# Kernel optimization log

Measured on AMD Instinct MI355X. Metric: run time of the kernel, lower is better.

## Reference

```python
import jax, jax.numpy as jnp
import numpy as np

BS = 8192
NUM_CLASSES = 400
D = 768


def _bilin_from_14(m14, Y, X, eH, eW):
    # Value of bilinear-resize(m14 -> (eH,eW)) at integer pixel (Y,X), computed on the fly.
    # torch F.interpolate(align_corners=False): src = (dst+0.5)*in/out - 0.5, clamped at 0.
    # m14: (bs,14,14); Y,X: (bs,14) float integer-valued coords; eH,eW: (bs,) float.
    sy = jnp.maximum((Y + 0.5) * 14.0 / eH[:, None] - 0.5, 0.0)
    sx = jnp.maximum((X + 0.5) * 14.0 / eW[:, None] - 0.5, 0.0)
    r0f = jnp.floor(sy); c0f = jnp.floor(sx)
    r0 = r0f.astype(jnp.int32); r1 = jnp.minimum(r0 + 1, 13)
    c0 = c0f.astype(jnp.int32); c1 = jnp.minimum(c0 + 1, 13)
    fy = sy - r0f; fx = sx - c0f
    b = jnp.arange(m14.shape[0])[:, None, None]
    g00 = m14[b, r0[:, :, None], c0[:, None, :]]
    g01 = m14[b, r0[:, :, None], c1[:, None, :]]
    g10 = m14[b, r1[:, :, None], c0[:, None, :]]
    g11 = m14[b, r1[:, :, None], c1[:, None, :]]
    wy = fy[:, :, None]; wx = fx[:, None, :]
    return g00 * (1 - wy) * (1 - wx) + g01 * (1 - wy) * wx + g10 * wy * (1 - wx) + g11 * wy * wx


def _get_mask(attn, o_pos, e_pos):
    # Fused, fully-batched equivalent of the per-sample python loop:
    #   resize 14x14 -> (eH,eW) bilinear; crop (top,left,oH,oW); resize -> 14x14 bilinear.
    # The final resize only reads the intermediate grid at 4 integer points per output
    # pixel, so we evaluate those points lazily via _bilin_from_14 (exact, no Emax grid).
    bs = attn.shape[0]
    m14 = attn.reshape(bs, 14, 14)
    eH = e_pos[:, 2].astype(jnp.float32); eW = e_pos[:, 3].astype(jnp.float32)
    top = (o_pos[:, 0] - e_pos[:, 0]).astype(jnp.float32)
    left = (o_pos[:, 1] - e_pos[:, 1]).astype(jnp.float32)
    oH = o_pos[:, 2].astype(jnp.float32); oW = o_pos[:, 3].astype(jnp.float32)
    i = jnp.arange(14, dtype=jnp.float32)[None, :]
    ty = jnp.maximum((i + 0.5) * oH[:, None] / 14.0 - 0.5, 0.0)  # (bs,14) coords in crop
    tx = jnp.maximum((i + 0.5) * oW[:, None] / 14.0 - 0.5, 0.0)
    y0 = jnp.floor(ty); y1 = jnp.minimum(y0 + 1.0, oH[:, None] - 1.0); wy = ty - y0
    x0 = jnp.floor(tx); x1 = jnp.minimum(x0 + 1.0, oW[:, None] - 1.0); wx = tx - x0
    Y0 = top[:, None] + y0; Y1 = top[:, None] + y1  # absolute rows in (eH,eW) grid
    X0 = left[:, None] + x0; X1 = left[:, None] + x1
    v00 = _bilin_from_14(m14, Y0, X0, eH, eW)
    v01 = _bilin_from_14(m14, Y0, X1, eH, eW)
    v10 = _bilin_from_14(m14, Y1, X0, eH, eW)
    v11 = _bilin_from_14(m14, Y1, X1, eH, eW)
    wyc = wy[:, :, None]; wxc = wx[:, None, :]
    out = v00 * (1 - wyc) * (1 - wxc) + v01 * (1 - wyc) * wxc + v10 * wyc * (1 - wxc) + v11 * wyc * wxc
    return out.reshape(bs, 196)


def _get_att_mask(attention, ratio=0.5):
    bs = attention.shape[0]
    a14 = attention.reshape(bs, 14, 14)
    # bilinear 14->7 with align_corners=False samples at frac 0.5 == 2x2 average pool
    a7 = a14.reshape(bs, 7, 2, 7, 2).mean(axis=(2, 4))
    flat = a7.reshape(bs, 49)
    n_keep = int(49 * ratio) + 1  # argsort desc, take top N+1 = 25
    _, idx = jax.lax.top_k(flat, n_keep)
    masks = jnp.ones((bs, 49), dtype=bool)
    masks = masks.at[jnp.arange(bs)[:, None], idx].set(False)
    m7 = masks.reshape(bs, 7, 7)
    full = jnp.repeat(jnp.repeat(m7, 2, axis=1), 2, axis=2)
    return full.reshape(bs, 196)


def setup_inputs() -> dict:
    key = jax.random.key(0)
    k1, k2, k3 = jax.random.split(key, 3)
    attn = jax.random.uniform(k1, (BS, 196), dtype=jnp.float32)
    rng = np.random.default_rng(0)
    IMG = 224
    eH = rng.integers(112, IMG + 1, BS); eW = rng.integers(112, IMG + 1, BS)
    eT = rng.integers(0, IMG - eH + 1); eL = rng.integers(0, IMG - eW + 1)
    def box():
        h = rng.integers(56, eH + 1); w = rng.integers(56, eW + 1)
        t = eT + rng.integers(0, eH - h + 1); l = eL + rng.integers(0, eW - w + 1)
        return np.stack([t, l, h, w], axis=1)
    e = np.stack([eT, eL, eH, eW], axis=1)
    pos = np.stack([box(), box(), e], axis=1).astype(np.int32)  # (BS,3,4)
    image_embed = jax.random.normal(k2, (2 * BS, D), dtype=jnp.float32)
    W = jax.random.normal(k3, (NUM_CLASSES, D), dtype=jnp.float32) * 0.02
    b = jnp.zeros((NUM_CLASSES,), dtype=jnp.float32)
    return {"attn": attn, "pos": jnp.asarray(pos), "image_embed": image_embed, "W": W, "b": b}


def reference(attn, pos, image_embed, W, b):
    cm1 = _get_mask(attn, pos[:, 0], pos[:, 2])
    mask1 = _get_att_mask(cm1)
    cm2 = _get_mask(attn, pos[:, 1], pos[:, 2])
    mask2 = _get_att_mask(cm2)
    mask = jnp.concatenate([mask1, mask2], axis=0)  # (2*bs,196) bool, fed to masked encoder
    logits = image_embed @ W.T + b
    return logits, mask
```

## Files before the change

### kernel.cpp

```cpp
#include <hip/hip_runtime.h>
#include <hip/hip_bf16.h>
#include <stdint.h>
#include <type_traits>

#define BSAMP 8192
#define NCLS 400
#define DIM 768
#define LOGITS_SIZE (16384LL * 400LL)
#define GEMM_BLOCKS 640
#define MASK_BLOCKS 4096
#define W_ELEMS (NCLS * DIM)

typedef __attribute__((ext_vector_type(8))) short short8;
typedef __attribute__((ext_vector_type(4))) float floatx4;

__device__ inline unsigned int packbf(float a, float b) {
    unsigned int ua = __float_as_uint(a) + 0x8000u;
    unsigned int ub = __float_as_uint(b) + 0x8000u;
    return __builtin_amdgcn_perm(ub, ua, 0x07060302u);
}

__device__ inline short8 cvt8(float4 lo, float4 hi) {
    union { unsigned int u[4]; short8 s; } r;
    r.u[0] = packbf(lo.x, lo.y);
    r.u[1] = packbf(lo.z, lo.w);
    r.u[2] = packbf(hi.x, hi.y);
    r.u[3] = packbf(hi.z, hi.w);
    return r.s;
}

__device__ inline void gload16(const void* g, void* l) {
    __builtin_amdgcn_global_load_lds((const __attribute__((address_space(1))) void*)g,
                                     (__attribute__((address_space(3))) void*)l, 16, 0, 0);
}

__global__ void cvtW_kernel(const float* __restrict__ W, unsigned short* __restrict__ ws) {
    int i = (blockIdx.x * 256 + threadIdx.x) * 4;
    if (i < W_ELEMS) {
        float4 f = *(const float4*)(W + i);
        uint2 r;
        r.x = packbf(f.x, f.y);
        r.y = packbf(f.z, f.w);
        *(uint2*)(ws + i) = r;
    }
}

__device__ inline float bilin14(const float* m14, float Y, float X, float eH, float eW) {
    float sy = fmaxf((Y + 0.5f) * 14.0f / eH - 0.5f, 0.0f);
    float sx = fmaxf((X + 0.5f) * 14.0f / eW - 0.5f, 0.0f);
    float r0f = floorf(sy);
    float c0f = floorf(sx);
    int r0 = (int)r0f;
    int r1 = min(r0 + 1, 13);
    int c0 = (int)c0f;
    int c1 = min(c0 + 1, 13);
    float fy = sy - r0f;
    float fx = sx - c0f;
    float g00 = m14[r0 * 14 + c0];
    float g01 = m14[r0 * 14 + c1];
    float g10 = m14[r1 * 14 + c0];
    float g11 = m14[r1 * 14 + c1];
    return g00 * (1.f - fy) * (1.f - fx) + g01 * (1.f - fy) * fx +
           g10 * fy * (1.f - fx) + g11 * fy * fx;
}

struct MaskSm { float m14[4][208]; float a7[4][56]; float mv[4][56]; };

template <bool USE_WS>
struct GemmSm {
    float A[2][128 * 32];
    typename std::conditional<USE_WS, unsigned short, float>::type B[2][80 * 32];
};

template <bool USE_WS>
__global__ __launch_bounds__(256, 2) void fused_kernel(const float* __restrict__ attn,
                                                       const int* __restrict__ pos,
                                                       const float* __restrict__ E,
                                                       const float* __restrict__ W,
                                                       const float* __restrict__ bias,
                                                       const unsigned short* __restrict__ wsW,
                                                       float* __restrict__ out) {
    __shared__ __align__(16) union SmU {
        GemmSm<USE_WS> g;
        MaskSm m;
    } sm;

    const int bx = blockIdx.x;
    const int t  = threadIdx.x;
    const int wv = t >> 6, ln = t & 63;

    if (bx < GEMM_BLOCKS) {
        const int xcd = bx & 7, li = bx >> 3;
        const int band = (li / 5) * 8 + xcd;
        const int n0 = (li % 5) * 80;
        const int m0 = band << 7;
        const int quad = ln >> 4, l16 = ln & 15;

        auto stageA = [&](int k0, float* buf) {
#pragma unroll
            for (int j = 0; j < 4; ++j) {
                int r = wv * 32 + j * 8 + (ln >> 3);
                int c = ln & 7;
                const float* src = E + (size_t)(m0 + r) * DIM + k0 + 4 * (c ^ (r & 7));
                gload16(src, buf + (wv * 32 + j * 8) * 32);
            }
        };
        auto stageBw = [&](int k0, unsigned short* buf) {
            for (int j = wv; j < 5; j += 4) {
                int row = j * 16 + (ln >> 2);
                int c = ln & 3;
                const unsigned short* src = wsW + (size_t)(n0 + row) * DIM + k0 + 8 * (c ^ ((row >> 1) & 3));
                gload16(src, buf + (j * 16) * 32);
            }
        };
        auto stageBf = [&](int k0, float* buf) {
            for (int j = wv; j < 10; j += 4) {
                int r = j * 8 + (ln >> 3);
                int c = ln & 7;
                const float* src = W + (size_t)(n0 + r) * DIM + k0 + 4 * (c ^ (r & 7));
                gload16(src, buf + (j * 8) * 32);
            }
        };
        auto stage = [&](int k0, int buf) {
            stageA(k0, sm.g.A[buf]);
            if constexpr (USE_WS) stageBw(k0, sm.g.B[buf]);
            else stageBf(k0, (float*)sm.g.B[buf]);
        };

        floatx4 acc[2][5];
#pragma unroll
        for (int mi = 0; mi < 2; ++mi)
#pragma unroll
            for (int ni = 0; ni < 5; ++ni)
                acc[mi][ni] = (floatx4){0.f, 0.f, 0.f, 0.f};

        stage(0, 0);
        stage(32, 1);
        __syncthreads();

        for (int it = 0; it < 24; ++it) {
            const int cur = it & 1;
            const float* aS = sm.g.A[cur];

            short8 af[2];
#pragma unroll
            for (int mi = 0; mi < 2; ++mi) {
                int r = wv * 32 + mi * 16 + l16;
                int rx = r & 7;
                const float* rp = aS + r * 32;
                float4 lo = *(const float4*)(rp + (((quad << 1) ^ rx) << 2));
                float4 hi = *(const float4*)(rp + ((((quad << 1) | 1) ^ rx) << 2));
                af[mi] = cvt8(lo, hi);
            }
#pragma unroll
            for (int ni = 0; ni < 5; ++ni) {
                int row = ni * 16 + l16;
                short8 bfr;
                if constexpr (USE_WS) {
                    bfr = *(const short8*)(sm.g.B[cur] + row * 32 + 8 * (quad ^ ((row >> 1) & 3)));
                } else {
                    int rx = row & 7;
                    const float* rp = (const float*)sm.g.B[cur] + row * 32;
                    float4 lo = *(const float4*)(rp + (((quad << 1) ^ rx) << 2));
                    float4 hi = *(const float4*)(rp + ((((quad << 1) | 1) ^ rx) << 2));
                    bfr = cvt8(lo, hi);
                }
                acc[0][ni] = __builtin_amdgcn_mfma_f32_16x16x32_bf16(af[0], bfr, acc[0][ni], 0, 0, 0);
                acc[1][ni] = __builtin_amdgcn_mfma_f32_16x16x32_bf16(af[1], bfr, acc[1][ni], 0, 0, 0);
            }

            __syncthreads();
            if (it < 22) stage((it + 2) * 32, cur);
        }

#pragma unroll
        for (int ni = 0; ni < 5; ++ni) {
            int col = n0 + ni * 16 + l16;
            float bv = bias[col];
#pragma unroll
            for (int mi = 0; mi < 2; ++mi) {
                int rowBase = m0 + wv * 32 + mi * 16 + quad * 4;
#pragma unroll
                for (int r = 0; r < 4; ++r) {
                    out[(size_t)(rowBase + r) * NCLS + col] = acc[mi][ni][r] + bv;
                }
            }
        }
    } else {
        const int p = (bx - GEMM_BLOCKS) * 4 + wv;
        const int b = p & (BSAMP - 1);
        const int o = p >> 13;
        float* m14 = sm.m.m14[wv];

        for (int i = ln; i < 196; i += 64) m14[i] = attn[(size_t)b * 196 + i];

        const int* pb = pos + (size_t)b * 12;
        const float topf  = (float)(pb[o * 4 + 0] - pb[8]);
        const float leftf = (float)(pb[o * 4 + 1] - pb[9]);
        const float oH = (float)pb[o * 4 + 2];
        const float oW = (float)pb[o * 4 + 3];
        const float eH = (float)pb[10];
        const float eW = (float)pb[11];
        __syncthreads();

        const int i7 = ln / 7, j7 = ln - i7 * 7;
        if (ln < 49) {
            float s = 0.f;
#pragma unroll
            for (int dy = 0; dy < 2; ++dy) {
                int oy = 2 * i7 + dy;
                float ty = fmaxf((oy + 0.5f) * oH / 14.0f - 0.5f, 0.0f);
                float y0 = floorf(ty);
                float y1 = fminf(y0 + 1.0f, oH - 1.0f);
                float wy = ty - y0;
                float Y0 = topf + y0, Y1 = topf + y1;
#pragma unroll
                for (int dx = 0; dx < 2; ++dx) {
                    int ox = 2 * j7 + dx;
                    float tx = fmaxf((ox + 0.5f) * oW / 14.0f - 0.5f, 0.0f);
                    float x0 = floorf(tx);
                    float x1 = fminf(x0 + 1.0f, oW - 1.0f);
                    float wx = tx - x0;
                    float X0 = leftf + x0, X1 = leftf + x1;
                    float v00 = bilin14(m14, Y0, X0, eH, eW);
                    float v01 = bilin14(m14, Y0, X1, eH, eW);
                    float v10 = bilin14(m14, Y1, X0, eH, eW);
                    float v11 = bilin14(m14, Y1, X1, eH, eW);
                    float cm = v00 * (1.f - wy) * (1.f - wx) + v01 * (1.f - wy) * wx +
                               v10 * wy * (1.f - wx) + v11 * wy * wx;
                    s += cm;
                }
            }
            sm.m.a7[wv][ln] = s * 0.25f;
        }
        __syncthreads();

        if (ln < 49) {
            float mine = sm.m.a7[wv][ln];
            int cnt = 0;
#pragma unroll 7
            for (int s2 = 0; s2 < 49; ++s2) {
                float v = sm.m.a7[wv][s2];
                cnt += (v > mine) || (v == mine && s2 < ln);
            }
            sm.m.mv[wv][ln] = (cnt < 25) ? 0.0f : 1.0f;
        }
        __syncthreads();

        float* ob = out + LOGITS_SIZE + (size_t)p * 196;
        for (int i = ln; i < 196; i += 64) {
            int oy = i / 14, ox = i - oy * 14;
            ob[i] = sm.m.mv[wv][(oy >> 1) * 7 + (ox >> 1)];
        }
    }
}

extern "C" void kernel_launch(void* const* d_in, const int* in_sizes, int n_in,
                              void* d_out, int out_size, void* d_ws, size_t ws_size,
                              hipStream_t stream) {
    const float* attn = (const float*)d_in[0];
    const int*   pos  = (const int*)d_in[1];
    const float* E    = (const float*)d_in[2];
    const float* W    = (const float*)d_in[3];
    const float* bias = (const float*)d_in[4];
    float* out = (float*)d_out;

    if (ws_size >= (size_t)W_ELEMS * 2) {
        unsigned short* ws = (unsigned short*)d_ws;
        cvtW_kernel<<<300, 256, 0, stream>>>(W, ws);
        fused_kernel<true><<<GEMM_BLOCKS + MASK_BLOCKS, 256, 0, stream>>>(
            attn, pos, E, W, bias, ws, out);
    } else {
        fused_kernel<false><<<GEMM_BLOCKS + MASK_BLOCKS, 256, 0, stream>>>(
            attn, pos, E, W, bias, nullptr, out);
    }
}
```

Baseline: 150.7 us.

## Halve GEMM tile rows to 64 for higher occupancy and hoist mask coordinate math

After: 150.0 us. Within noise of the previous version (-0.5%).

```diff
diff --git a/kernel.cpp b/kernel.cpp
--- a/kernel.cpp
+++ b/kernel.cpp
@@ -7,7 +7,7 @@
 #define NCLS 400
 #define DIM 768
 #define LOGITS_SIZE (16384LL * 400LL)
-#define GEMM_BLOCKS 640
+#define GEMM_BLOCKS 1280
 #define MASK_BLOCKS 4096
 #define W_ELEMS (NCLS * DIM)
 
@@ -45,17 +45,9 @@
     }
 }
 
-__device__ inline float bilin14(const float* m14, float Y, float X, float eH, float eW) {
-    float sy = fmaxf((Y + 0.5f) * 14.0f / eH - 0.5f, 0.0f);
-    float sx = fmaxf((X + 0.5f) * 14.0f / eW - 0.5f, 0.0f);
-    float r0f = floorf(sy);
-    float c0f = floorf(sx);
-    int r0 = (int)r0f;
+__device__ inline float tap4(const float* m14, int r0, int c0, float fy, float fx) {
     int r1 = min(r0 + 1, 13);
-    int c0 = (int)c0f;
     int c1 = min(c0 + 1, 13);
-    float fy = sy - r0f;
-    float fx = sx - c0f;
     float g00 = m14[r0 * 14 + c0];
     float g01 = m14[r0 * 14 + c1];
     float g10 = m14[r1 * 14 + c0];
@@ -68,12 +60,12 @@
 
 template <bool USE_WS>
 struct GemmSm {
-    float A[2][128 * 32];
+    float A[2][64 * 32];
     typename std::conditional<USE_WS, unsigned short, float>::type B[2][80 * 32];
 };
 
 template <bool USE_WS>
-__global__ __launch_bounds__(256, 2) void fused_kernel(const float* __restrict__ attn,
+__global__ __launch_bounds__(256, 6) void fused_kernel(const float* __restrict__ attn,
                                                        const int* __restrict__ pos,
                                                        const float* __restrict__ E,
                                                        const float* __restrict__ W,
@@ -90,19 +82,17 @@
     const int wv = t >> 6, ln = t & 63;
 
     if (bx < GEMM_BLOCKS) {
-        const int xcd = bx & 7, li = bx >> 3;
-        const int band = (li / 5) * 8 + xcd;
-        const int n0 = (li % 5) * 80;
-        const int m0 = band << 7;
+        const int n0 = (bx % 5) * 80;
+        const int m0 = (bx / 5) * 64;
         const int quad = ln >> 4, l16 = ln & 15;
 
         auto stageA = [&](int k0, float* buf) {
 #pragma unroll
-            for (int j = 0; j < 4; ++j) {
-                int r = wv * 32 + j * 8 + (ln >> 3);
+            for (int j = 0; j < 2; ++j) {
+                int r = wv * 16 + j * 8 + (ln >> 3);
                 int c = ln & 7;
                 const float* src = E + (size_t)(m0 + r) * DIM + k0 + 4 * (c ^ (r & 7));
-                gload16(src, buf + (wv * 32 + j * 8) * 32);
+                gload16(src, buf + (wv * 16 + j * 8) * 32);
             }
         };
         auto stageBw = [&](int k0, unsigned short* buf) {
@@ -127,12 +117,9 @@
             else stageBf(k0, (float*)sm.g.B[buf]);
         };
 
-        floatx4 acc[2][5];
-#pragma unroll
-        for (int mi = 0; mi < 2; ++mi)
-#pragma unroll
-            for (int ni = 0; ni < 5; ++ni)
-                acc[mi][ni] = (floatx4){0.f, 0.f, 0.f, 0.f};
+        floatx4 acc[5];
+#pragma unroll
+        for (int ni = 0; ni < 5; ++ni) acc[ni] = (floatx4){0.f, 0.f, 0.f, 0.f};
 
         stage(0, 0);
         stage(32, 1);
@@ -140,17 +127,14 @@
 
         for (int it = 0; it < 24; ++it) {
             const int cur = it & 1;
-            const float* aS = sm.g.A[cur];
-
-            short8 af[2];
-#pragma unroll
-            for (int mi = 0; mi < 2; ++mi) {
-                int r = wv * 32 + mi * 16 + l16;
-                int rx = r & 7;
-                const float* rp = aS + r * 32;
+
+            short8 af;
+            {
+                int rx = l16 & 7;
+                const float* rp = sm.g.A[cur] + (wv * 16 + l16) * 32;
                 float4 lo = *(const float4*)(rp + (((quad << 1) ^ rx) << 2));
                 float4 hi = *(const float4*)(rp + ((((quad << 1) | 1) ^ rx) << 2));
-                af[mi] = cvt8(lo, hi);
+                af = cvt8(lo, hi);
             }
 #pragma unroll
             for (int ni = 0; ni < 5; ++ni) {
@@ -165,25 +149,21 @@
                     float4 hi = *(const float4*)(rp + ((((quad << 1) | 1) ^ rx) << 2));
                     bfr = cvt8(lo, hi);
                 }
-                acc[0][ni] = __builtin_amdgcn_mfma_f32_16x16x32_bf16(af[0], bfr, acc[0][ni], 0, 0, 0);
-                acc[1][ni] = __builtin_amdgcn_mfma_f32_16x16x32_bf16(af[1], bfr, acc[1][ni], 0, 0, 0);
+                acc[ni] = __builtin_amdgcn_mfma_f32_16x16x32_bf16(af, bfr, acc[ni], 0, 0, 0);
             }
 
             __syncthreads();
             if (it < 22) stage((it + 2) * 32, cur);
         }
 
+        const int rowBase = m0 + wv * 16 + quad * 4;
 #pragma unroll
         for (int ni = 0; ni < 5; ++ni) {
             int col = n0 + ni * 16 + l16;
             float bv = bias[col];
 #pragma unroll
-            for (int mi = 0; mi < 2; ++mi) {
-                int rowBase = m0 + wv * 32 + mi * 16 + quad * 4;
-#pragma unroll
-                for (int r = 0; r < 4; ++r) {
-                    out[(size_t)(rowBase + r) * NCLS + col] = acc[mi][ni][r] + bv;
-                }
+            for (int r = 0; r < 4; ++r) {
+                out[(size_t)(rowBase + r) * NCLS + col] = acc[ni][r] + bv;
             }
         }
     } else {
@@ -205,27 +185,50 @@
 
         const int i7 = ln / 7, j7 = ln - i7 * 7;
         if (ln < 49) {
-            float s = 0.f;
+            int   cI[2][2];  float cF[2][2];  float wxs[2];
+            int   rI[2][2];  float rF[2][2];  float wys[2];
+#pragma unroll
+            for (int dx = 0; dx < 2; ++dx) {
+                int ox = 2 * j7 + dx;
+                float tx = fmaxf((ox + 0.5f) * oW / 14.0f - 0.5f, 0.0f);
+                float x0 = floorf(tx);
+                float x1 = fminf(x0 + 1.0f, oW - 1.0f);
+                wxs[dx] = tx - x0;
+                float X0 = leftf + x0, X1 = leftf + x1;
+                float sx0 = fmaxf((X0 + 0.5f) * 14.0f / eW - 0.5f, 0.0f);
+                float c0f = floorf(sx0);
+                cI[dx][0] = (int)c0f; cF[dx][0] = sx0 - c0f;
+                float sx1 = fmaxf((X1 + 0.5f) * 14.0f / eW - 0.5f, 0.0f);
+                float c1f = floorf(sx1);
+                cI[dx][1] = (int)c1f; cF[dx][1] = sx1 - c1f;
+            }
 #pragma unroll
             for (int dy = 0; dy < 2; ++dy) {
                 int oy = 2 * i7 + dy;
                 float ty = fmaxf((oy + 0.5f) * oH / 14.0f - 0.5f, 0.0f);
                 float y0 = floorf(ty);
                 float y1 = fminf(y0 + 1.0f, oH - 1.0f);
-                float wy = ty - y0;
+                wys[dy] = ty - y0;
                 float Y0 = topf + y0, Y1 = topf + y1;
+                float sy0 = fmaxf((Y0 + 0.5f) * 14.0f / eH - 0.5f, 0.0f);
+                float r0f = floorf(sy0);
+                rI[dy][0] = (int)r0f; rF[dy][0] = sy0 - r0f;
+                float sy1 = fmaxf((Y1 + 0.5f) * 14.0f / eH - 0.5f, 0.0f);
+                float r1f = floorf(sy1);
+                rI[dy][1] = (int)r1f; rF[dy][1] = sy1 - r1f;
+            }
+
+            float s = 0.f;
+#pragma unroll
+            for (int dy = 0; dy < 2; ++dy) {
+                float wy = wys[dy];
 #pragma unroll
                 for (int dx = 0; dx < 2; ++dx) {
-                    int ox = 2 * j7 + dx;
-                    float tx = fmaxf((ox + 0.5f) * oW / 14.0f - 0.5f, 0.0f);
-                    float x0 = floorf(tx);
-                    float x1 = fminf(x0 + 1.0f, oW - 1.0f);
-                    float wx = tx - x0;
-                    float X0 = leftf + x0, X1 = leftf + x1;
-                    float v00 = bilin14(m14, Y0, X0, eH, eW);
-                    float v01 = bilin14(m14, Y0, X1, eH, eW);
-                    float v10 = bilin14(m14, Y1, X0, eH, eW);
-                    float v11 = bilin14(m14, Y1, X1, eH, eW);
+                    float wx = wxs[dx];
+                    float v00 = tap4(m14, rI[dy][0], cI[dx][0], rF[dy][0], cF[dx][0]);
+                    float v01 = tap4(m14, rI[dy][0], cI[dx][1], rF[dy][0], cF[dx][1]);
+                    float v10 = tap4(m14, rI[dy][1], cI[dx][0], rF[dy][1], cF[dx][0]);
+                    float v11 = tap4(m14, rI[dy][1], cI[dx][1], rF[dy][1], cF[dx][1]);
                     float cm = v00 * (1.f - wy) * (1.f - wx) + v01 * (1.f - wy) * wx +
                                v10 * wy * (1.f - wx) + v11 * wy * wx;
                     s += cm;
```
